# Kernel optimization log

Measured on AMD Instinct MI355X. Metric: run time of the kernel, lower is better.

## Reference

```python
import jax, jax.numpy as jnp
import numpy as np

N_NODES = 50000
N_EDGES = 600000
D = 128


def setup_inputs() -> dict:
    key = jax.random.key(0)
    ks = jax.random.split(key, 8)
    x = jax.random.normal(ks[0], (N_NODES, D), dtype=jnp.float32)
    edge_index = jax.random.randint(ks[1], (2, N_EDGES), 0, N_NODES, dtype=jnp.int64)
    s = 1.0 / np.sqrt(D)
    W_l1 = jax.random.uniform(ks[2], (D, D), jnp.float32, -s, s)
    W_r1 = jax.random.uniform(ks[3], (D, D), jnp.float32, -s, s)
    b1 = jnp.zeros((D,), jnp.float32)
    W_l2 = jax.random.uniform(ks[4], (D, D), jnp.float32, -s, s)
    W_r2 = jax.random.uniform(ks[5], (D, D), jnp.float32, -s, s)
    b2 = jnp.zeros((D,), jnp.float32)
    return {"x": x, "edge_index": edge_index, "W_l1": W_l1, "W_r1": W_r1,
            "b1": b1, "W_l2": W_l2, "W_r2": W_r2, "b2": b2}


def _sage_conv(x, src, dst, W_l, W_r, b):
    # mean aggregation over incoming edges (src -> dst), PyG SAGEConv semantics
    n = x.shape[0]
    msg = x[src]                                               # [E, D] gather
    agg = jax.ops.segment_sum(msg, dst, num_segments=n)        # [N, D] scatter-add
    cnt = jax.ops.segment_sum(jnp.ones((src.shape[0],), x.dtype), dst, num_segments=n)
    mean = agg / jnp.maximum(cnt, 1.0)[:, None]
    return mean @ W_l + x @ W_r + b


def reference(x, edge_index, W_l1, W_r1, b1, W_l2, W_r2, b2):
    src, dst = edge_index[0], edge_index[1]
    h = jax.nn.relu(_sage_conv(x, src, dst, W_l1, W_r1, b1))
    out = _sage_conv(h, src, dst, W_l2, W_r2, b2)
    return out
```

## Files before the change

kernel.cpp:

```cpp
#include <hip/hip_runtime.h>
#include <hip/hip_bf16.h>

#define N_NODES 50000
#define N_EDGES 600000
#define D 128
#define K2 256
#define MAXDEG 64

#define CVT_BLOCKS   (N_NODES * 16 / 256)
#define BUILD_BLOCKS ((N_EDGES / 4 + 255) / 256)
#define PREPW_BLOCKS (2 * D * K2 / 256)
#define PREP_GRID (CVT_BLOCKS + BUILD_BLOCKS + PREPW_BLOCKS)

typedef __bf16 bf16x8 __attribute__((ext_vector_type(8)));
typedef float  f32x16 __attribute__((ext_vector_type(16)));

__device__ __forceinline__ unsigned short f32_to_bf16_rne(float f) {
    unsigned int u = __builtin_bit_cast(unsigned int, f);
    unsigned int r = (u + 0x7fffu + ((u >> 16) & 1u)) >> 16;
    return (unsigned short)r;
}
__device__ __forceinline__ unsigned pk2(float lo, float hi) {
    return (unsigned)f32_to_bf16_rne(lo) | ((unsigned)f32_to_bf16_rne(hi) << 16);
}
__device__ __forceinline__ float bfl(unsigned int u) { return __builtin_bit_cast(float, u << 16); }
__device__ __forceinline__ float bfh(unsigned int u) { return __builtin_bit_cast(float, u & 0xffff0000u); }

__global__ __launch_bounds__(256) void prep_kernel(
    const float* __restrict__ x, const int* __restrict__ ei,
    const float* __restrict__ Wl1, const float* __restrict__ Wr1,
    const float* __restrict__ Wl2, const float* __restrict__ Wr2,
    unsigned short* __restrict__ A0, unsigned short* __restrict__ WT,
    int* __restrict__ counts, int* __restrict__ slots)
{
    const int b = blockIdx.x;
    if (b < CVT_BLOCKS) {
        int idx = b * 256 + threadIdx.x;
        int node = idx >> 4, g = idx & 15;
        const float4* xp = (const float4*)(x + (size_t)node * D + g * 8);
        float4 v0 = xp[0], v1 = xp[1];
        uint4 o;
        o.x = pk2(v0.x, v0.y); o.y = pk2(v0.z, v0.w);
        o.z = pk2(v1.x, v1.y); o.w = pk2(v1.z, v1.w);
        ((uint4*)A0)[(size_t)node * 16 + g] = o;
    } else if (b < CVT_BLOCKS + BUILD_BLOCKS) {
        int e4 = ((b - CVT_BLOCKS) * 256 + threadIdx.x) * 4;
        if (e4 < N_EDGES) {
            int4 s4 = *(const int4*)(ei + e4);
            int4 d4 = *(const int4*)(ei + N_EDGES + e4);
            int p0 = atomicAdd(&counts[d4.x], 1);
            int p1 = atomicAdd(&counts[d4.y], 1);
            int p2 = atomicAdd(&counts[d4.z], 1);
            int p3 = atomicAdd(&counts[d4.w], 1);
            if (p0 < MAXDEG) slots[(size_t)d4.x * MAXDEG + p0] = s4.x;
            if (p1 < MAXDEG) slots[(size_t)d4.y * MAXDEG + p1] = s4.y;
            if (p2 < MAXDEG) slots[(size_t)d4.z * MAXDEG + p2] = s4.z;
            if (p3 < MAXDEG) slots[(size_t)d4.w * MAXDEG + p3] = s4.w;
        }
    } else {
        int idx = (b - CVT_BLOCKS - BUILD_BLOCKS) * 256 + threadIdx.x;
        int layer = idx >> 15, rem = idx & 32767;
        int n = rem >> 8, k = rem & 255;
        const float* Wl = layer ? Wl2 : Wl1;
        const float* Wr = layer ? Wr2 : Wr1;
        float v = (k < D) ? Wl[k * D + n] : Wr[(k - D) * D + n];
        WT[((size_t)layer << 15) + n * K2 + k] = f32_to_bf16_rne(v);
    }
}

template <bool RELU, bool OUT_BF16>
__global__ __launch_bounds__(256) void layer_kernel(
    const unsigned short* __restrict__ Xin,
    const int* __restrict__ counts, const int* __restrict__ slots,
    const unsigned short* __restrict__ WT,
    const float* __restrict__ bias,
    unsigned short* __restrict__ Hout,
    float* __restrict__ outf)
{
    __shared__ uint4 As4[32 * 33];
    const int tid = threadIdx.x;
    const int lane = tid & 63;
    const int wv = tid >> 6;
    const int base = blockIdx.x * 32;
    const int g = lane >> 4;
    const int u = lane & 15;
    const uint4* X4 = (const uint4*)Xin;

    const int nodeb = base + wv * 8;

    int cntv = 0;
    {
        int nn = nodeb + (lane & 7);
        if (nn < N_NODES) cntv = counts[nn];
    }
    int sreg[8];
    #pragma unroll
    for (int i = 0; i < 8; ++i) {
        int node = nodeb + i;
        sreg[i] = (node < N_NODES) ? slots[(size_t)node * MAXDEG + lane] : 0;
    }

    #pragma unroll
    for (int i = 0; i < 8; ++i) {
        const int m = wv * 8 + i;
        const int node = nodeb + i;
        int cnt = __builtin_amdgcn_readlane(cntv, i);
        cnt = cnt > MAXDEG ? MAXDEG : cnt;

        float a0 = 0.f, a1 = 0.f, a2 = 0.f, a3 = 0.f;
        float a4 = 0.f, a5 = 0.f, a6 = 0.f, a7 = 0.f;

        for (int e0 = 0; e0 < cnt; e0 += 16) {
            #pragma unroll
            for (int j = 0; j < 4; ++j) {
                int eidx = e0 + j * 4 + g;
                int s = __shfl(sreg[i], eidx, 64);
                uint4 v = {0u, 0u, 0u, 0u};
                if (eidx < cnt) v = X4[(size_t)s * 16 + u];
                a0 += bfl(v.x); a1 += bfh(v.x);
                a2 += bfl(v.y); a3 += bfh(v.y);
                a4 += bfl(v.z); a5 += bfh(v.z);
                a6 += bfl(v.w); a7 += bfh(v.w);
            }
        }

        a0 += __shfl_xor(a0, 16, 64); a1 += __shfl_xor(a1, 16, 64);
        a2 += __shfl_xor(a2, 16, 64); a3 += __shfl_xor(a3, 16, 64);
        a4 += __shfl_xor(a4, 16, 64); a5 += __shfl_xor(a5, 16, 64);
        a6 += __shfl_xor(a6, 16, 64); a7 += __shfl_xor(a7, 16, 64);
        a0 += __shfl_xor(a0, 32, 64); a1 += __shfl_xor(a1, 32, 64);
        a2 += __shfl_xor(a2, 32, 64); a3 += __shfl_xor(a3, 32, 64);
        a4 += __shfl_xor(a4, 32, 64); a5 += __shfl_xor(a5, 32, 64);
        a6 += __shfl_xor(a6, 32, 64); a7 += __shfl_xor(a7, 32, 64);

        const float inv = 1.0f / fmaxf((float)cnt, 1.0f);
        if (g == 0) {
            uint4 o;
            o.x = pk2(a0 * inv, a1 * inv); o.y = pk2(a2 * inv, a3 * inv);
            o.z = pk2(a4 * inv, a5 * inv); o.w = pk2(a6 * inv, a7 * inv);
            As4[u * 33 + m] = o;
        } else if (g == 1) {
            uint4 xv = {0u, 0u, 0u, 0u};
            if (node < N_NODES) xv = X4[(size_t)node * 16 + u];
            As4[(16 + u) * 33 + m] = xv;
        }
    }
    __syncthreads();

    const int m = lane & 31;
    const int kg = lane >> 5;
    const int col = wv * 32 + m;
    const uint4* bp = (const uint4*)(WT + (size_t)col * K2 + kg * 8);
    const bf16x8* afrag = (const bf16x8*)As4;

    f32x16 acc = {};
    #pragma unroll
    for (int s = 0; s < 16; ++s) {
        bf16x8 a = afrag[(s * 2 + kg) * 33 + m];
        bf16x8 b = __builtin_bit_cast(bf16x8, bp[s * 2]);
        acc = __builtin_amdgcn_mfma_f32_32x32x16_bf16(a, b, acc, 0, 0, 0);
    }

    const float bc = bias[col];
    const int halfadd = kg * 4;
    #pragma unroll
    for (int r = 0; r < 16; ++r) {
        int rw = base + (r & 3) + 8 * (r >> 2) + halfadd;
        if (rw < N_NODES) {
            float v = acc[r] + bc;
            if (RELU) v = fmaxf(v, 0.0f);
            if (OUT_BF16) Hout[(size_t)rw * D + col] = f32_to_bf16_rne(v);
            else outf[(size_t)rw * D + col] = v;
        }
    }
}

extern "C" void kernel_launch(void* const* d_in, const int* in_sizes, int n_in,
                              void* d_out, int out_size, void* d_ws, size_t ws_size,
                              hipStream_t stream) {
    const float* x   = (const float*)d_in[0];
    const int*   ei  = (const int*)d_in[1];
    const float* Wl1 = (const float*)d_in[2];
    const float* Wr1 = (const float*)d_in[3];
    const float* b1  = (const float*)d_in[4];
    const float* Wl2 = (const float*)d_in[5];
    const float* Wr2 = (const float*)d_in[6];
    const float* b2  = (const float*)d_in[7];
    float* out = (float*)d_out;

    unsigned short* A0 = (unsigned short*)d_ws;
    unsigned short* A1 = A0 + (size_t)N_NODES * D;
    unsigned short* WT = A1 + (size_t)N_NODES * D;
    int* counts = (int*)(WT + 2 * D * K2);
    int* slots  = counts + N_NODES;

    const int layerBlocks = (N_NODES + 31) / 32;

    hipMemsetAsync(counts, 0, N_NODES * sizeof(int), stream);
    prep_kernel<<<PREP_GRID, 256, 0, stream>>>(x, ei, Wl1, Wr1, Wl2, Wr2, A0, WT, counts, slots);

    layer_kernel<true, true><<<layerBlocks, 256, 0, stream>>>(
        A0, counts, slots, WT, b1, A1, nullptr);
    layer_kernel<false, false><<<layerBlocks, 256, 0, stream>>>(
        A1, counts, slots, WT + (size_t)D * K2, b2, nullptr, out);
}
```

Baseline: 194.9 us.

## Assign one node per 16-lane group in aggregation, removing cross-group reductions

The gather-aggregate phase is restructured so each 16-lane quarter-wave owns one destination node at a time (two nodes per group, four groups per wave) instead of all 64 lanes cooperating on a single node. This removes the shuffle-xor reductions and the per-node serial loop, unrolls the edge loop in 16-edge chunks gated by wave-wide any checks, and preloads self features. The prep kernel block order is also changed so edge-slot building blocks launch first. The new scheme adds divergence across groups with different degrees and serializes up to 16 dependent loads per lane per chunk.

```diff
diff --git a/kernel.cpp b/kernel.cpp
--- a/kernel.cpp
+++ b/kernel.cpp
@@ -7,10 +7,10 @@
 #define K2 256
 #define MAXDEG 64
 
+#define BUILD_BLOCKS ((N_EDGES / 4 + 255) / 256)
 #define CVT_BLOCKS   (N_NODES * 16 / 256)
-#define BUILD_BLOCKS ((N_EDGES / 4 + 255) / 256)
 #define PREPW_BLOCKS (2 * D * K2 / 256)
-#define PREP_GRID (CVT_BLOCKS + BUILD_BLOCKS + PREPW_BLOCKS)
+#define PREP_GRID (BUILD_BLOCKS + CVT_BLOCKS + PREPW_BLOCKS)
 
 typedef __bf16 bf16x8 __attribute__((ext_vector_type(8)));
 typedef float  f32x16 __attribute__((ext_vector_type(16)));
@@ -34,17 +34,8 @@
     int* __restrict__ counts, int* __restrict__ slots)
 {
     const int b = blockIdx.x;
-    if (b < CVT_BLOCKS) {
-        int idx = b * 256 + threadIdx.x;
-        int node = idx >> 4, g = idx & 15;
-        const float4* xp = (const float4*)(x + (size_t)node * D + g * 8);
-        float4 v0 = xp[0], v1 = xp[1];
-        uint4 o;
-        o.x = pk2(v0.x, v0.y); o.y = pk2(v0.z, v0.w);
-        o.z = pk2(v1.x, v1.y); o.w = pk2(v1.z, v1.w);
-        ((uint4*)A0)[(size_t)node * 16 + g] = o;
-    } else if (b < CVT_BLOCKS + BUILD_BLOCKS) {
-        int e4 = ((b - CVT_BLOCKS) * 256 + threadIdx.x) * 4;
+    if (b < BUILD_BLOCKS) {
+        int e4 = (b * 256 + threadIdx.x) * 4;
         if (e4 < N_EDGES) {
             int4 s4 = *(const int4*)(ei + e4);
             int4 d4 = *(const int4*)(ei + N_EDGES + e4);
@@ -57,8 +48,17 @@
             if (p2 < MAXDEG) slots[(size_t)d4.z * MAXDEG + p2] = s4.z;
             if (p3 < MAXDEG) slots[(size_t)d4.w * MAXDEG + p3] = s4.w;
         }
+    } else if (b < BUILD_BLOCKS + CVT_BLOCKS) {
+        int idx = (b - BUILD_BLOCKS) * 256 + threadIdx.x;
+        int node = idx >> 4, g = idx & 15;
+        const float4* xp = (const float4*)(x + (size_t)node * D + g * 8);
+        float4 v0 = xp[0], v1 = xp[1];
+        uint4 o;
+        o.x = pk2(v0.x, v0.y); o.y = pk2(v0.z, v0.w);
+        o.z = pk2(v1.x, v1.y); o.w = pk2(v1.z, v1.w);
+        ((uint4*)A0)[(size_t)node * 16 + g] = o;
     } else {
-        int idx = (b - CVT_BLOCKS - BUILD_BLOCKS) * 256 + threadIdx.x;
+        int idx = (b - BUILD_BLOCKS - CVT_BLOCKS) * 256 + threadIdx.x;
         int layer = idx >> 15, rem = idx & 32767;
         int n = rem >> 8, k = rem & 255;
         const float* Wl = layer ? Wl2 : Wl1;
@@ -85,66 +85,71 @@
     const int g = lane >> 4;
     const int u = lane & 15;
     const uint4* X4 = (const uint4*)Xin;
-
     const int nodeb = base + wv * 8;
 
-    int cntv = 0;
-    {
-        int nn = nodeb + (lane & 7);
-        if (nn < N_NODES) cntv = counts[nn];
-    }
-    int sreg[8];
-    #pragma unroll
-    for (int i = 0; i < 8; ++i) {
-        int node = nodeb + i;
-        sreg[i] = (node < N_NODES) ? slots[(size_t)node * MAXDEG + lane] : 0;
-    }
-
-    #pragma unroll
-    for (int i = 0; i < 8; ++i) {
-        const int m = wv * 8 + i;
-        const int node = nodeb + i;
-        int cnt = __builtin_amdgcn_readlane(cntv, i);
-        cnt = cnt > MAXDEG ? MAXDEG : cnt;
-
+    const int n0 = nodeb + g;
+    const int n1 = nodeb + 4 + g;
+    const bool ok0 = n0 < N_NODES, ok1 = n1 < N_NODES;
+
+    int cnt0 = 0, cnt1 = 0;
+    if (ok0) cnt0 = counts[n0];
+    if (ok1) cnt1 = counts[n1];
+
+    int sreg[2][4];
+    #pragma unroll
+    for (int r = 0; r < 4; ++r) {
+        sreg[0][r] = ok0 ? slots[(size_t)n0 * MAXDEG + r * 16 + u] : 0;
+        sreg[1][r] = ok1 ? slots[(size_t)n1 * MAXDEG + r * 16 + u] : 0;
+    }
+
+    uint4 xv0 = {0u,0u,0u,0u}, xv1 = {0u,0u,0u,0u};
+    if (ok0) xv0 = X4[(size_t)n0 * 16 + u];
+    if (ok1) xv1 = X4[(size_t)n1 * 16 + u];
+
+    cnt0 = cnt0 > MAXDEG ? MAXDEG : cnt0;
+    cnt1 = cnt1 > MAXDEG ? MAXDEG : cnt1;
+
+    #pragma unroll
+    for (int s = 0; s < 2; ++s) {
+        const int m = wv * 8 + s * 4 + g;
+        const int cnt = s ? cnt1 : cnt0;
         float a0 = 0.f, a1 = 0.f, a2 = 0.f, a3 = 0.f;
         float a4 = 0.f, a5 = 0.f, a6 = 0.f, a7 = 0.f;
 
-        for (int e0 = 0; e0 < cnt; e0 += 16) {
-            #pragma unroll
-            for (int j = 0; j < 4; ++j) {
-                int eidx = e0 + j * 4 + g;
-                int s = __shfl(sreg[i], eidx, 64);
-                uint4 v = {0u, 0u, 0u, 0u};
-                if (eidx < cnt) v = X4[(size_t)s * 16 + u];
-                a0 += bfl(v.x); a1 += bfh(v.x);
-                a2 += bfl(v.y); a3 += bfh(v.y);
-                a4 += bfl(v.z); a5 += bfh(v.z);
-                a6 += bfl(v.w); a7 += bfh(v.w);
+        #pragma unroll
+        for (int e = 0; e < 16; ++e) {
+            int idx = __shfl(sreg[s][0], g * 16 + e, 64);
+            if (e < cnt) {
+                uint4 v = X4[(size_t)idx * 16 + u];
+                a0 += bfl(v.x); a1 += bfh(v.x); a2 += bfl(v.y); a3 += bfh(v.y);
+                a4 += bfl(v.z); a5 += bfh(v.z); a6 += bfl(v.w); a7 += bfh(v.w);
             }
         }
-
-        a0 += __shfl_xor(a0, 16, 64); a1 += __shfl_xor(a1, 16, 64);
-        a2 += __shfl_xor(a2, 16, 64); a3 += __shfl_xor(a3, 16, 64);
-        a4 += __shfl_xor(a4, 16, 64); a5 += __shfl_xor(a5, 16, 64);
-        a6 += __shfl_xor(a6, 16, 64); a7 += __shfl_xor(a7, 16, 64);
-        a0 += __shfl_xor(a0, 32, 64); a1 += __shfl_xor(a1, 32, 64);
-        a2 += __shfl_xor(a2, 32, 64); a3 += __shfl_xor(a3, 32, 64);
-        a4 += __shfl_xor(a4, 32, 64); a5 += __shfl_xor(a5, 32, 64);
-        a6 += __shfl_xor(a6, 32, 64); a7 += __shfl_xor(a7, 32, 64);
+        #pragma unroll
+        for (int r = 1; r < 4; ++r) {
+            if (__any(cnt > r * 16)) {
+                #pragma unroll
+                for (int e = 0; e < 16; ++e) {
+                    int idx = __shfl(sreg[s][r], g * 16 + e, 64);
+                    if (r * 16 + e < cnt) {
+                        uint4 v = X4[(size_t)idx * 16 + u];
+                        a0 += bfl(v.x); a1 += bfh(v.x); a2 += bfl(v.y); a3 += bfh(v.y);
+                        a4 += bfl(v.z); a5 += bfh(v.z); a6 += bfl(v.w); a7 += bfh(v.w);
+                    }
+                }
+            }
+        }
 
         const float inv = 1.0f / fmaxf((float)cnt, 1.0f);
-        if (g == 0) {
-            uint4 o;
-            o.x = pk2(a0 * inv, a1 * inv); o.y = pk2(a2 * inv, a3 * inv);
-            o.z = pk2(a4 * inv, a5 * inv); o.w = pk2(a6 * inv, a7 * inv);
-            As4[u * 33 + m] = o;
-        } else if (g == 1) {
-            uint4 xv = {0u, 0u, 0u, 0u};
-            if (node < N_NODES) xv = X4[(size_t)node * 16 + u];
-            As4[(16 + u) * 33 + m] = xv;
-        }
-    }
+        uint4 o;
+        o.x = pk2(a0 * inv, a1 * inv); o.y = pk2(a2 * inv, a3 * inv);
+        o.z = pk2(a4 * inv, a5 * inv); o.w = pk2(a6 * inv, a7 * inv);
+        As4[u * 33 + m] = o;
+    }
+
+    As4[(16 + u) * 33 + (wv * 8 + g)]     = xv0;
+    As4[(16 + u) * 33 + (wv * 8 + 4 + g)] = xv1;
+
     __syncthreads();
 
     const int m = lane & 31;
```

Measured after the change: 230.9 us. +18.4%, slower.
